# Performance work log

Hardware: AMD Instinct MI355X
Metric: run time of the kernel (lower is better)

Reference implementation:

```python
import jax, jax.numpy as jnp
import numpy as np
from jax import lax

# Dims matching init_kwargs
T, BK, OBS = 2048, 64, 64   # obs_dim = percept_dim(63) + reward_dim(1)
H, P, N = 16, 64, 64        # nheads, headdim, d_state; d_inner = H*P = 1024
DIN = H * P


def setup_inputs() -> dict:
    key = jax.random.key(0)
    ks = jax.random.split(key, 12)
    s = lambda fan_in: 1.0 / np.sqrt(fan_in)
    return {
        "obs": jax.random.normal(ks[0], (T, BK, OBS), jnp.float32),
        "reward": jax.random.normal(ks[1], (T, BK, 1), jnp.float32),
        "W_in": jax.random.normal(ks[2], (OBS, DIN), jnp.float32) * s(OBS),
        "W_B": jax.random.normal(ks[3], (OBS, N), jnp.float32) * s(OBS),
        "W_C": jax.random.normal(ks[4], (OBS, N), jnp.float32) * s(OBS),
        "W_dt": jax.random.normal(ks[5], (1, H), jnp.float32),
        "dt_bias": jax.random.normal(ks[6], (H,), jnp.float32) * 0.5,
        "A_log": jax.random.uniform(ks[7], (H,), jnp.float32, 0.0, 1.0),
        "D": jax.random.normal(ks[8], (H,), jnp.float32),
        "W_out": jax.random.normal(ks[9], (DIN, 1), jnp.float32) * s(DIN),
        "init_state": jax.random.normal(ks[10], (H, P, N), jnp.float32) * 0.1,
        "k": 8,
    }


def reference(obs, reward, W_in, W_B, W_C, W_dt, dt_bias, A_log, D, W_out, init_state, k):
    # obs: (T, Bk, obs_dim), reward: (T, Bk, 1)
    Tn, Bk, _ = obs.shape
    # Precompute per-step projections (vectorized over time)
    u = (obs @ W_in).reshape(Tn, Bk, H, P)      # (T,Bk,H,P) input stream
    Bm = obs @ W_B                              # (T,Bk,N) input-dependent B
    Cm = obs @ W_C                              # (T,Bk,N) input-dependent C
    dt = jax.nn.softplus(reward @ W_dt + dt_bias)  # (T,Bk,H) reward-modulated dt
    A = -jnp.exp(A_log)                          # (H,) negative decay rates
    decay = jnp.exp(dt * A)                     # (T,Bk,H)

    # Cache init: zeros + initial_states (per QAgent.forward)
    h0 = jnp.broadcast_to(init_state, (Bk, H, P, N))

    def step(h, inp):
        u_t, B_t, C_t, dt_t, dec_t = inp
        # selective-scan state update: h = h*exp(dt*A) + dt*u (outer) B
        h = h * dec_t[..., None, None] + (dt_t[..., None] * u_t)[..., None] * B_t[:, None, None, :]
        y = jnp.einsum('bhpn,bn->bhp', h, C_t) + D[None, :, None] * u_t
        o = y.reshape(Bk, DIN) @ W_out          # (Bk, 1) scalar Q per option
        return h, o

    _, ys = lax.scan(step, h0, (u, Bm, Cm, dt, decay))  # ys: (T, Bk, 1)
    q = ys.reshape(Tn, -1, k)                   # (T, B, k)
    logits = q
    return q, logits
```

## Files before the change

### kernel.cpp

```cpp
#include <hip/hip_runtime.h>
#include <math.h>

#define TT     2048
#define BKK    64
#define OBSD   64
#define NH     16
#define PDIM   64
#define NSTATE 64
#define DINN   1024
#define TB     (TT*BKK)
#define NC     32
#define CL     (TT/NC)

#define RS      164
#define OFF_C   64
#define OFF_DEC 128
#define OFF_XW  144
#define OFF_OB  160

template <int CTRL>
__device__ __forceinline__ float dpp_add(float x) {
    int y = __builtin_amdgcn_update_dpp(0, __float_as_int(x), CTRL, 0xF, 0xF, true);
    return x + __int_as_float(y);
}
__device__ __forceinline__ float wave_sum_lane63(float x) {
    x = dpp_add<0x111>(x);
    x = dpp_add<0x112>(x);
    x = dpp_add<0x114>(x);
    x = dpp_add<0x118>(x);
    x = dpp_add<0x142>(x);
    x = dpp_add<0x143>(x);
    return x;
}

__device__ __forceinline__ float softplusf(float z) {
    return (z > 20.f) ? z : log1pf(expf(z));
}

__global__ void dup_q(float* __restrict__ q) {
    int i = blockIdx.x * 256 + threadIdx.x;
    if (i < TB) q[TB + i] = q[i];
}

__global__ __launch_bounds__(1024)
void init_proj(const float* __restrict__ Win, const float* __restrict__ Wout,
               const float* __restrict__ initS,
               float* __restrict__ wproj, float* __restrict__ g0) {
    const int tid = threadIdx.x;
    {
        const int k = tid >> 4, h = tid & 15;
        float s = 0.f;
#pragma unroll 8
        for (int p = 0; p < PDIM; ++p)
            s = fmaf(Win[(size_t)k * DINN + h * 64 + p], Wout[h * 64 + p], s);
        wproj[tid] = s;
    }
    {
        const int h = tid >> 6, n = tid & 63;
        float s = 0.f;
#pragma unroll 8
        for (int p = 0; p < PDIM; ++p)
            s = fmaf(initS[h * PDIM * NSTATE + p * NSTATE + n], Wout[h * 64 + p], s);
        g0[tid] = s;
    }
}

__global__ __launch_bounds__(256)
void prelude2(const float* __restrict__ obs, const float* __restrict__ reward,
              const float* __restrict__ WB, const float* __restrict__ WC,
              const float* __restrict__ Wdt, const float* __restrict__ dtb,
              const float* __restrict__ Alog, const float* __restrict__ Dv,
              const float* __restrict__ wproj, float* __restrict__ rows) {
    int gw = (blockIdx.x * 256 + threadIdx.x) >> 6;
    gw = __builtin_amdgcn_readfirstlane(gw);
    const int lane = threadIdx.x & 63;
    const int row0 = gw * 8;
    if (row0 >= TB) return;

    const int h = lane & 15;
    const int q = lane >> 4;

    const float wdt_h = Wdt[h];
    const float dtb_h = dtb[h];
    const float A_h   = -expf(Alog[h]);
    const float D_h   = Dv[h];
    float wpj[16];
#pragma unroll
    for (int j = 0; j < 16; ++j)
        wpj[j] = wproj[(q * 16 + j) * 16 + h];

    float aB[8], aC[8];
#pragma unroll
    for (int r = 0; r < 8; ++r) { aB[r] = 0.f; aC[r] = 0.f; }
#pragma unroll 8
    for (int kk = 0; kk < OBSD; ++kk) {
        float wb = WB[kk * 64 + lane];
        float wc = WC[kk * 64 + lane];
#pragma unroll
        for (int r = 0; r < 8; ++r) {
            float o = obs[(size_t)(row0 + r) * OBSD + kk];
            aB[r] = fmaf(o, wb, aB[r]);
            aC[r] = fmaf(o, wc, aC[r]);
        }
    }

#pragma unroll 1
    for (int r = 0; r < 8; ++r) {
        const int row = row0 + r;
        float* rb = rows + (size_t)row * RS;
        rb[lane]         = aB[r];
        rb[OFF_C + lane] = aC[r];

        const float4* oq = (const float4*)(obs + (size_t)row * OBSD + q * 16);
        float4 o0 = oq[0], o1 = oq[1], o2 = oq[2], o3 = oq[3];
        float wpart = 0.f;
        wpart = fmaf(o0.x, wpj[0],  wpart); wpart = fmaf(o0.y, wpj[1],  wpart);
        wpart = fmaf(o0.z, wpj[2],  wpart); wpart = fmaf(o0.w, wpj[3],  wpart);
        wpart = fmaf(o1.x, wpj[4],  wpart); wpart = fmaf(o1.y, wpj[5],  wpart);
        wpart = fmaf(o1.z, wpj[6],  wpart); wpart = fmaf(o1.w, wpj[7],  wpart);
        wpart = fmaf(o2.x, wpj[8],  wpart); wpart = fmaf(o2.y, wpj[9],  wpart);
        wpart = fmaf(o2.z, wpj[10], wpart); wpart = fmaf(o2.w, wpj[11], wpart);
        wpart = fmaf(o3.x, wpj[12], wpart); wpart = fmaf(o3.y, wpj[13], wpart);
        wpart = fmaf(o3.z, wpj[14], wpart); wpart = fmaf(o3.w, wpj[15], wpart);
        wpart += __shfl_xor(wpart, 16, 64);
        wpart += __shfl_xor(wpart, 32, 64);

        const float rew  = reward[row];
        const float dtv  = softplusf(fmaf(rew, wdt_h, dtb_h));
        const float decv = expf(dtv * A_h);
        const float xwv  = dtv * wpart;
        if (q == 0) rb[OFF_DEC + h] = decv;
        if (q == 1) rb[OFF_XW  + h] = xwv;

        float dw = D_h * wpart;
        dw += __shfl_xor(dw, 1, 64);
        dw += __shfl_xor(dw, 2, 64);
        dw += __shfl_xor(dw, 4, 64);
        dw += __shfl_xor(dw, 8, 64);
        if (lane == 0) rb[OFF_OB] = dw;
    }
}

__global__ __launch_bounds__(256)
void phaseA(const float* __restrict__ rows, float* __restrict__ Send,
            float* __restrict__ Ptot) {
    int w = (blockIdx.x * 256 + threadIdx.x) >> 6;
    w = __builtin_amdgcn_readfirstlane(w);
    const int lane = threadIdx.x & 63;
    const int b = w & 63;
    const int c = w >> 6;

    const float* rowp = rows + ((size_t)(c * CL) * BKK + b) * RS;
    float g[16], Pc[16];
#pragma unroll
    for (int hh = 0; hh < 16; ++hh) { g[hh] = 0.f; Pc[hh] = 1.f; }

    float Bv = rowp[lane];

#pragma unroll 2
    for (int i = 0; i < CL; ++i) {
        const float* nxt = rowp + (size_t)RS * BKK;
        float Bn = 0.f;
        if (i < CL - 1) Bn = nxt[lane];
#pragma unroll
        for (int hh = 0; hh < 16; ++hh) {
            const float dh = rowp[OFF_DEC + hh];
            g[hh] = fmaf(g[hh], dh, rowp[OFF_XW + hh] * Bv);
            Pc[hh] *= dh;
        }
        rowp = nxt; Bv = Bn;
    }

    const size_t base = ((size_t)c * BKK + b) * 16;
#pragma unroll
    for (int hh = 0; hh < 16; ++hh)
        Send[(base + hh) * 64 + lane] = g[hh];
    if (lane == 0) {
#pragma unroll
        for (int hh = 0; hh < 16; ++hh)
            Ptot[base + hh] = Pc[hh];
    }
}

__global__ __launch_bounds__(64)
void phaseB(const float* __restrict__ g0, const float* __restrict__ Send,
            const float* __restrict__ Ptot, float* __restrict__ gcbuf) {
    const int b    = blockIdx.x;
    const int lane = threadIdx.x;

    float g[16];
#pragma unroll
    for (int hh = 0; hh < 16; ++hh)
        g[hh] = g0[hh * 64 + lane];

#pragma unroll 1
    for (int c = 0; c < NC; ++c) {
        const size_t base = ((size_t)c * BKK + b) * 16;
#pragma unroll
        for (int hh = 0; hh < 16; ++hh)
            gcbuf[(base + hh) * 64 + lane] = g[hh];
        if (c < NC - 1) {
#pragma unroll
            for (int hh = 0; hh < 16; ++hh)
                g[hh] = fmaf(Ptot[base + hh], g[hh], Send[(base + hh) * 64 + lane]);
        }
    }
}

__global__ __launch_bounds__(256)
void phaseC(const float* __restrict__ rows, const float* __restrict__ gcbuf,
            float* __restrict__ qout) {
    int w = (blockIdx.x * 256 + threadIdx.x) >> 6;
    w = __builtin_amdgcn_readfirstlane(w);
    const int lane = threadIdx.x & 63;
    const int b = w & 63;
    const int c = w >> 6;

    const size_t base = ((size_t)c * BKK + b) * 16;
    float g[16];
#pragma unroll
    for (int hh = 0; hh < 16; ++hh)
        g[hh] = gcbuf[(base + hh) * 64 + lane];

    const float* rowp = rows + ((size_t)(c * CL) * BKK + b) * RS;
    float Bv = rowp[lane];
    float Cv = rowp[OFF_C + lane];

#pragma unroll 2
    for (int i = 0; i < CL; ++i) {
        const float* nxt = rowp + (size_t)RS * BKK;
        float Bn = 0.f, Cn = 0.f;
        if (i < CL - 1) { Bn = nxt[lane]; Cn = nxt[OFF_C + lane]; }

        float y = 0.f;
#pragma unroll
        for (int hh = 0; hh < 16; ++hh) {
            g[hh] = fmaf(g[hh], rowp[OFF_DEC + hh], rowp[OFF_XW + hh] * Bv);
            y = fmaf(g[hh], Cv, y);
        }
        const float ob = rowp[OFF_OB];

        float tot = wave_sum_lane63(y);
        if (lane == 63) qout[(size_t)(c * CL + i) * BKK + b] = tot + ob;

        rowp = nxt; Bv = Bn; Cv = Cn;
    }
}

__global__ __launch_bounds__(64)
void scan3_kernel(const float* __restrict__ rows, const float* __restrict__ g0,
                  float* __restrict__ qout) {
    const int b    = blockIdx.x;
    const int lane = threadIdx.x;

    float g[16];
#pragma unroll
    for (int hh = 0; hh < 16; ++hh)
        g[hh] = g0[hh * 64 + lane];

    const float* rowp = rows + (size_t)b * RS;
    float Bv = rowp[lane];
    float Cv = rowp[OFF_C + lane];

#pragma unroll 2
    for (int t = 0; t < TT; ++t) {
        const float* nrow = rowp + (size_t)RS * BKK;
        float Bn = 0.f, Cn = 0.f;
        if (t < TT - 1) { Bn = nrow[lane]; Cn = nrow[OFF_C + lane]; }

        float y = 0.f;
#pragma unroll
        for (int hh = 0; hh < 16; ++hh) {
            float tmp = rowp[OFF_XW + hh] * Bv;
            g[hh] = fmaf(g[hh], rowp[OFF_DEC + hh], tmp);
            y = fmaf(g[hh], Cv, y);
        }
        const float ob = rowp[OFF_OB];

        float tot = wave_sum_lane63(y);
        if (lane == 63) qout[(size_t)t * BKK + b] = tot + ob;

        rowp = nrow; Bv = Bn; Cv = Cn;
    }
}

extern "C" void kernel_launch(void* const* d_in, const int* in_sizes, int n_in,
                              void* d_out, int out_size, void* d_ws, size_t ws_size,
                              hipStream_t stream) {
    const float* obs    = (const float*)d_in[0];
    const float* reward = (const float*)d_in[1];
    const float* Win    = (const float*)d_in[2];
    const float* WB     = (const float*)d_in[3];
    const float* WC     = (const float*)d_in[4];
    const float* Wdt    = (const float*)d_in[5];
    const float* dtb    = (const float*)d_in[6];
    const float* Alog   = (const float*)d_in[7];
    const float* Dv     = (const float*)d_in[8];
    const float* Wout   = (const float*)d_in[9];
    const float* initS  = (const float*)d_in[10];
    float* qout = (float*)d_out;

    const size_t n_rows = (size_t)TB * RS;
    const size_t n_cs   = (size_t)NC * BKK * 16 * 64;
    const size_t n_pt   = (size_t)NC * BKK * 16;

    const size_t need1 = (n_rows + 2048) * 4;
    const size_t need2 = (n_rows + 2048 + 2 * n_cs + n_pt) * 4;

    float* rows  = (float*)d_ws;
    float* wproj = rows + n_rows;
    float* g0    = wproj + 1024;

    if (ws_size >= need2) {
        float* Send  = g0 + 1024;
        float* gcbuf = Send + n_cs;
        float* Ptot  = gcbuf + n_cs;
        hipLaunchKernelGGL(init_proj, dim3(1),        dim3(1024), 0, stream,
                           Win, Wout, initS, wproj, g0);
        hipLaunchKernelGGL(prelude2,  dim3(TB / 32),  dim3(256),  0, stream,
                           obs, reward, WB, WC, Wdt, dtb, Alog, Dv, wproj, rows);
        hipLaunchKernelGGL(phaseA,    dim3(512),      dim3(256),  0, stream,
                           rows, Send, Ptot);
        hipLaunchKernelGGL(phaseB,    dim3(BKK),      dim3(64),   0, stream,
                           g0, Send, Ptot, gcbuf);
        hipLaunchKernelGGL(phaseC,    dim3(512),      dim3(256),  0, stream,
                           rows, gcbuf, qout);
        hipLaunchKernelGGL(dup_q,     dim3(TB / 256), dim3(256),  0, stream, qout);
    } else {
        hipLaunchKernelGGL(init_proj, dim3(1),        dim3(1024), 0, stream,
                           Win, Wout, initS, wproj, g0);
        hipLaunchKernelGGL(prelude2,  dim3(TB / 32),  dim3(256),  0, stream,
                           obs, reward, WB, WC, Wdt, dtb, Alog, Dv, wproj, rows);
        hipLaunchKernelGGL(scan3_kernel, dim3(BKK),   dim3(64),   0, stream,
                           rows, g0, qout);
        hipLaunchKernelGGL(dup_q,     dim3(TB / 256), dim3(256),  0, stream, qout);
    }
}
```

Baseline: 256.1 us.

## Parallelize init, stage obs in LDS, prefetch scan rows, double chunks, fuse dup

init_proj is spread over 8 blocks instead of one 1024-thread block. prelude2 now stages its obs rows in LDS once rather than reading them repeatedly from global memory. phaseA, phaseB and phaseC prefetch the next row's decay and xw values (and phaseB the next chunk's state) as float4 loads into registers to hide load latency. When the workspace allows, the chunk count doubles to 64, which halves each sequential chunk and doubles phaseA/C parallelism at the cost of a longer phaseB carry chain. phaseC writes both output copies directly, which removes the dup_q launch.

```diff
diff --git a/kernel.cpp b/kernel.cpp
--- a/kernel.cpp
+++ b/kernel.cpp
@@ -9,8 +9,6 @@
 #define NSTATE 64
 #define DINN   1024
 #define TB     (TT*BKK)
-#define NC     32
-#define CL     (TT/NC)
 
 #define RS      164
 #define OFF_C   64
@@ -42,26 +40,27 @@
     if (i < TB) q[TB + i] = q[i];
 }
 
-__global__ __launch_bounds__(1024)
-void init_proj(const float* __restrict__ Win, const float* __restrict__ Wout,
-               const float* __restrict__ initS,
-               float* __restrict__ wproj, float* __restrict__ g0) {
-    const int tid = threadIdx.x;
-    {
-        const int k = tid >> 4, h = tid & 15;
+__global__ __launch_bounds__(256)
+void init_proj2(const float* __restrict__ Win, const float* __restrict__ Wout,
+                const float* __restrict__ initS,
+                float* __restrict__ wproj, float* __restrict__ g0) {
+    const int t = threadIdx.x;
+    if (blockIdx.x < 4) {
+        const int idx = blockIdx.x * 256 + t;
+        const int k = idx >> 4, h = idx & 15;
         float s = 0.f;
 #pragma unroll 8
         for (int p = 0; p < PDIM; ++p)
             s = fmaf(Win[(size_t)k * DINN + h * 64 + p], Wout[h * 64 + p], s);
-        wproj[tid] = s;
-    }
-    {
-        const int h = tid >> 6, n = tid & 63;
+        wproj[idx] = s;
+    } else {
+        const int idx = (blockIdx.x - 4) * 256 + t;
+        const int h = idx >> 6, n = idx & 63;
         float s = 0.f;
 #pragma unroll 8
         for (int p = 0; p < PDIM; ++p)
             s = fmaf(initS[h * PDIM * NSTATE + p * NSTATE + n], Wout[h * 64 + p], s);
-        g0[tid] = s;
+        g0[idx] = s;
     }
 }
 
@@ -71,12 +70,26 @@
               const float* __restrict__ Wdt, const float* __restrict__ dtb,
               const float* __restrict__ Alog, const float* __restrict__ Dv,
               const float* __restrict__ wproj, float* __restrict__ rows) {
-    int gw = (blockIdx.x * 256 + threadIdx.x) >> 6;
-    gw = __builtin_amdgcn_readfirstlane(gw);
-    const int lane = threadIdx.x & 63;
-    const int row0 = gw * 8;
-    if (row0 >= TB) return;
-
+    __shared__ float lds[4][64][10];
+
+    const int t    = threadIdx.x;
+    const int lane = t & 63;
+    const int wv   = t >> 6;
+    const int row0b = blockIdx.x * 32;
+
+    {
+        const float4* op4 = (const float4*)(obs + (size_t)row0b * OBSD) + t * 2;
+        float4 v0 = op4[0], v1 = op4[1];
+        const int rb = t >> 3;
+        const int r  = rb & 7;
+        const int c0 = (t & 7) * 8;
+        lds[wv][c0 + 0][r] = v0.x; lds[wv][c0 + 1][r] = v0.y;
+        lds[wv][c0 + 2][r] = v0.z; lds[wv][c0 + 3][r] = v0.w;
+        lds[wv][c0 + 4][r] = v1.x; lds[wv][c0 + 5][r] = v1.y;
+        lds[wv][c0 + 6][r] = v1.z; lds[wv][c0 + 7][r] = v1.w;
+    }
+
+    const int row0 = row0b + wv * 8;
     const int h = lane & 15;
     const int q = lane >> 4;
 
@@ -92,16 +105,22 @@
     float aB[8], aC[8];
 #pragma unroll
     for (int r = 0; r < 8; ++r) { aB[r] = 0.f; aC[r] = 0.f; }
-#pragma unroll 8
+
+    const float* base = &lds[wv][0][0];
+#pragma unroll 4
     for (int kk = 0; kk < OBSD; ++kk) {
+        const float2* pr = (const float2*)(base + kk * 10);
+        float2 p0 = pr[0], p1 = pr[1], p2 = pr[2], p3 = pr[3];
         float wb = WB[kk * 64 + lane];
         float wc = WC[kk * 64 + lane];
-#pragma unroll
-        for (int r = 0; r < 8; ++r) {
-            float o = obs[(size_t)(row0 + r) * OBSD + kk];
-            aB[r] = fmaf(o, wb, aB[r]);
-            aC[r] = fmaf(o, wc, aC[r]);
-        }
+        aB[0] = fmaf(p0.x, wb, aB[0]);  aC[0] = fmaf(p0.x, wc, aC[0]);
+        aB[1] = fmaf(p0.y, wb, aB[1]);  aC[1] = fmaf(p0.y, wc, aC[1]);
+        aB[2] = fmaf(p1.x, wb, aB[2]);  aC[2] = fmaf(p1.x, wc, aC[2]);
+        aB[3] = fmaf(p1.y, wb, aB[3]);  aC[3] = fmaf(p1.y, wc, aC[3]);
+        aB[4] = fmaf(p2.x, wb, aB[4]);  aC[4] = fmaf(p2.x, wc, aC[4]);
+        aB[5] = fmaf(p2.y, wb, aB[5]);  aC[5] = fmaf(p2.y, wc, aC[5]);
+        aB[6] = fmaf(p3.x, wb, aB[6]);  aC[6] = fmaf(p3.x, wc, aC[6]);
+        aB[7] = fmaf(p3.y, wb, aB[7]);  aC[7] = fmaf(p3.y, wc, aC[7]);
     }
 
 #pragma unroll 1
@@ -141,10 +160,26 @@
     }
 }
 
+#define LOAD_DX(ptr, dd, xx)                                              \
+    {                                                                     \
+        const float4* _p = (const float4*)((ptr) + OFF_DEC);              \
+        float4 a0 = _p[0], a1 = _p[1], a2 = _p[2], a3 = _p[3];            \
+        float4 b0 = _p[4], b1 = _p[5], b2 = _p[6], b3 = _p[7];            \
+        dd[0]=a0.x; dd[1]=a0.y; dd[2]=a0.z; dd[3]=a0.w;                   \
+        dd[4]=a1.x; dd[5]=a1.y; dd[6]=a1.z; dd[7]=a1.w;                   \
+        dd[8]=a2.x; dd[9]=a2.y; dd[10]=a2.z; dd[11]=a2.w;                 \
+        dd[12]=a3.x; dd[13]=a3.y; dd[14]=a3.z; dd[15]=a3.w;               \
+        xx[0]=b0.x; xx[1]=b0.y; xx[2]=b0.z; xx[3]=b0.w;                   \
+        xx[4]=b1.x; xx[5]=b1.y; xx[6]=b1.z; xx[7]=b1.w;                   \
+        xx[8]=b2.x; xx[9]=b2.y; xx[10]=b2.z; xx[11]=b2.w;                 \
+        xx[12]=b3.x; xx[13]=b3.y; xx[14]=b3.z; xx[15]=b3.w;               \
+    }
+
+template <int CL>
 __global__ __launch_bounds__(256)
 void phaseA(const float* __restrict__ rows, float* __restrict__ Send,
             float* __restrict__ Ptot) {
-    int w = (blockIdx.x * 256 + threadIdx.x) >> 6;
+    int w = blockIdx.x * 4 + (threadIdx.x >> 6);
     w = __builtin_amdgcn_readfirstlane(w);
     const int lane = threadIdx.x & 63;
     const int b = w & 63;
@@ -156,19 +191,28 @@
     for (int hh = 0; hh < 16; ++hh) { g[hh] = 0.f; Pc[hh] = 1.f; }
 
     float Bv = rowp[lane];
+    float dec_[16], xw_[16];
+    LOAD_DX(rowp, dec_, xw_);
 
 #pragma unroll 2
     for (int i = 0; i < CL; ++i) {
         const float* nxt = rowp + (size_t)RS * BKK;
         float Bn = 0.f;
-        if (i < CL - 1) Bn = nxt[lane];
+        float decn_[16], xwn_[16];
+        if (i < CL - 1) {
+            Bn = nxt[lane];
+            LOAD_DX(nxt, decn_, xwn_);
+        }
 #pragma unroll
         for (int hh = 0; hh < 16; ++hh) {
-            const float dh = rowp[OFF_DEC + hh];
-            g[hh] = fmaf(g[hh], dh, rowp[OFF_XW + hh] * Bv);
-            Pc[hh] *= dh;
+            g[hh] = fmaf(g[hh], dec_[hh], xw_[hh] * Bv);
+            Pc[hh] *= dec_[hh];
         }
         rowp = nxt; Bv = Bn;
+        if (i < CL - 1) {
+#pragma unroll
+            for (int hh = 0; hh < 16; ++hh) { dec_[hh] = decn_[hh]; xw_[hh] = xwn_[hh]; }
+        }
     }
 
     const size_t base = ((size_t)c * BKK + b) * 16;
@@ -182,9 +226,11 @@
     }
 }
 
+template <int CL>
 __global__ __launch_bounds__(64)
 void phaseB(const float* __restrict__ g0, const float* __restrict__ Send,
             const float* __restrict__ Ptot, float* __restrict__ gcbuf) {
+    const int NCv  = TT / CL;
     const int b    = blockIdx.x;
     const int lane = threadIdx.x;
 
@@ -193,57 +239,100 @@
     for (int hh = 0; hh < 16; ++hh)
         g[hh] = g0[hh * 64 + lane];
 
+    float S_[16], P_[16];
+    {
+        const size_t base = (size_t)b * 16;
+#pragma unroll
+        for (int hh = 0; hh < 16; ++hh) S_[hh] = Send[(base + hh) * 64 + lane];
+        const float4* pp = (const float4*)(Ptot + base);
+        float4 a0 = pp[0], a1 = pp[1], a2 = pp[2], a3 = pp[3];
+        P_[0]=a0.x; P_[1]=a0.y; P_[2]=a0.z; P_[3]=a0.w;
+        P_[4]=a1.x; P_[5]=a1.y; P_[6]=a1.z; P_[7]=a1.w;
+        P_[8]=a2.x; P_[9]=a2.y; P_[10]=a2.z; P_[11]=a2.w;
+        P_[12]=a3.x; P_[13]=a3.y; P_[14]=a3.z; P_[15]=a3.w;
+    }
+
 #pragma unroll 1
-    for (int c = 0; c < NC; ++c) {
-        const size_t base = ((size_t)c * BKK + b) * 16;
+    for (int c = 0; c < NCv; ++c) {
+        const size_t base  = ((size_t)c * BKK + b) * 16;
+        float Sn[16], Pn[16];
+        if (c < NCv - 1) {
+            const size_t nb = ((size_t)(c + 1) * BKK + b) * 16;
+#pragma unroll
+            for (int hh = 0; hh < 16; ++hh) Sn[hh] = Send[(nb + hh) * 64 + lane];
+            const float4* pp = (const float4*)(Ptot + nb);
+            float4 a0 = pp[0], a1 = pp[1], a2 = pp[2], a3 = pp[3];
+            Pn[0]=a0.x; Pn[1]=a0.y; Pn[2]=a0.z; Pn[3]=a0.w;
+            Pn[4]=a1.x; Pn[5]=a1.y; Pn[6]=a1.z; Pn[7]=a1.w;
+            Pn[8]=a2.x; Pn[9]=a2.y; Pn[10]=a2.z; Pn[11]=a2.w;
+            Pn[12]=a3.x; Pn[13]=a3.y; Pn[14]=a3.z; Pn[15]=a3.w;
+        }
 #pragma unroll
         for (int hh = 0; hh < 16; ++hh)
             gcbuf[(base + hh) * 64 + lane] = g[hh];
-        if (c < NC - 1) {
-#pragma unroll
-            for (int hh = 0; hh < 16; ++hh)
-                g[hh] = fmaf(Ptot[base + hh], g[hh], Send[(base + hh) * 64 + lane]);
-        }
-    }
-}
-
+        if (c < NCv - 1) {
+#pragma unroll
+            for (int hh = 0; hh < 16; ++hh) {
+                g[hh] = fmaf(P_[hh], g[hh], S_[hh]);
+                P_[hh] = Pn[hh]; S_[hh] = Sn[hh];
+            }
+        }
+    }
+}
+
+template <int CL>
 __global__ __launch_bounds__(256)
 void phaseC(const float* __restrict__ rows, const float* __restrict__ gcbuf,
             float* __restrict__ qout) {
-    int w = (blockIdx.x * 256 + threadIdx.x) >> 6;
+    int w = blockIdx.x * 4 + (threadIdx.x >> 6);
     w = __builtin_amdgcn_readfirstlane(w);
     const int lane = threadIdx.x & 63;
     const int b = w & 63;
     const int c = w >> 6;
 
-    const size_t base = ((size_t)c * BKK + b) * 16;
+    const size_t sbase = ((size_t)c * BKK + b) * 16;
     float g[16];
 #pragma unroll
     for (int hh = 0; hh < 16; ++hh)
-        g[hh] = gcbuf[(base + hh) * 64 + lane];
+        g[hh] = gcbuf[(sbase + hh) * 64 + lane];
 
     const float* rowp = rows + ((size_t)(c * CL) * BKK + b) * RS;
     float Bv = rowp[lane];
     float Cv = rowp[OFF_C + lane];
+    float ob = rowp[OFF_OB];
+    float dec_[16], xw_[16];
+    LOAD_DX(rowp, dec_, xw_);
 
 #pragma unroll 2
     for (int i = 0; i < CL; ++i) {
         const float* nxt = rowp + (size_t)RS * BKK;
-        float Bn = 0.f, Cn = 0.f;
-        if (i < CL - 1) { Bn = nxt[lane]; Cn = nxt[OFF_C + lane]; }
+        float Bn = 0.f, Cn = 0.f, obn = 0.f;
+        float decn_[16], xwn_[16];
+        if (i < CL - 1) {
+            Bn = nxt[lane]; Cn = nxt[OFF_C + lane]; obn = nxt[OFF_OB];
+            LOAD_DX(nxt, decn_, xwn_);
+        }
 
         float y = 0.f;
 #pragma unroll
         for (int hh = 0; hh < 16; ++hh) {
-            g[hh] = fmaf(g[hh], rowp[OFF_DEC + hh], rowp[OFF_XW + hh] * Bv);
+            g[hh] = fmaf(g[hh], dec_[hh], xw_[hh] * Bv);
             y = fmaf(g[hh], Cv, y);
         }
-        const float ob = rowp[OFF_OB];
 
         float tot = wave_sum_lane63(y);
-        if (lane == 63) qout[(size_t)(c * CL + i) * BKK + b] = tot + ob;
-
-        rowp = nxt; Bv = Bn; Cv = Cn;
+        if (lane == 63) {
+            const size_t idx = (size_t)(c * CL + i) * BKK + b;
+            const float v = tot + ob;
+            qout[idx]      = v;
+            qout[TB + idx] = v;
+        }
+
+        rowp = nxt; Bv = Bn; Cv = Cn; ob = obn;
+        if (i < CL - 1) {
+#pragma unroll
+            for (int hh = 0; hh < 16; ++hh) { dec_[hh] = decn_[hh]; xw_[hh] = xwn_[hh]; }
+        }
     }
 }
 
@@ -301,38 +390,39 @@
     float* qout = (float*)d_out;
 
     const size_t n_rows = (size_t)TB * RS;
-    const size_t n_cs   = (size_t)NC * BKK * 16 * 64;
-    const size_t n_pt   = (size_t)NC * BKK * 16;
-
-    const size_t need1 = (n_rows + 2048) * 4;
-    const size_t need2 = (n_rows + 2048 + 2 * n_cs + n_pt) * 4;
 
     float* rows  = (float*)d_ws;
     float* wproj = rows + n_rows;
     float* g0    = wproj + 1024;
 
-    if (ws_size >= need2) {
+    const size_t n_cs64 = (size_t)64 * BKK * 16 * 64;
+    const size_t n_pt64 = (size_t)64 * BKK * 16;
+    const size_t need64 = (n_rows + 2048 + 2 * n_cs64 + n_pt64) * 4;
+
+    const size_t n_cs32 = (size_t)32 * BKK * 16 * 64;
+    const size_t n_pt32 = (size_t)32 * BKK * 16;
+    const size_t need32 = (n_rows + 2048 + 2 * n_cs32 + n_pt32) * 4;
+
+    init_proj2<<<dim3(8), dim3(256), 0, stream>>>(Win, Wout, initS, wproj, g0);
+    prelude2<<<dim3(TB / 32), dim3(256), 0, stream>>>(obs, reward, WB, WC, Wdt,
+                                                      dtb, Alog, Dv, wproj, rows);
+
+    if (ws_size >= need64) {
         float* Send  = g0 + 1024;
-        float* gcbuf = Send + n_cs;
-        float* Ptot  = gcbuf + n_cs;
-        hipLaunchKernelGGL(init_proj, dim3(1),        dim3(1024), 0, stream,
-                           Win, Wout, initS, wproj, g0);
-        hipLaunchKernelGGL(prelude2,  dim3(TB / 32),  dim3(256),  0, stream,
-                           obs, reward, WB, WC, Wdt, dtb, Alog, Dv, wproj, rows);
-        hipLaunchKernelGGL(phaseA,    dim3(512),      dim3(256),  0, stream,
-                           rows, Send, Ptot);
-        hipLaunchKernelGGL(phaseB,    dim3(BKK),      dim3(64),   0, stream,
-                           g0, Send, Ptot, gcbuf);
-        hipLaunchKernelGGL(phaseC,    dim3(512),      dim3(256),  0, stream,
-                           rows, gcbuf, qout);
-        hipLaunchKernelGGL(dup_q,     dim3(TB / 256), dim3(256),  0, stream, qout);
+        float* gcbuf = Send + n_cs64;
+        float* Ptot  = gcbuf + n_cs64;
+        phaseA<32><<<dim3(64 * 16), dim3(256), 0, stream>>>(rows, Send, Ptot);
+        phaseB<32><<<dim3(BKK), dim3(64), 0, stream>>>(g0, Send, Ptot, gcbuf);
+        phaseC<32><<<dim3(64 * 16), dim3(256), 0, stream>>>(rows, gcbuf, qout);
+    } else if (ws_size >= need32) {
+        float* Send  = g0 + 1024;
+        float* gcbuf = Send + n_cs32;
+        float* Ptot  = gcbuf + n_cs32;
+        phaseA<64><<<dim3(32 * 16), dim3(256), 0, stream>>>(rows, Send, Ptot);
+        phaseB<64><<<dim3(BKK), dim3(64), 0, stream>>>(g0, Send, Ptot, gcbuf);
+        phaseC<64><<<dim3(32 * 16), dim3(256), 0, stream>>>(rows, gcbuf, qout);
     } else {
-        hipLaunchKernelGGL(init_proj, dim3(1),        dim3(1024), 0, stream,
-                           Win, Wout, initS, wproj, g0);
-        hipLaunchKernelGGL(prelude2,  dim3(TB / 32),  dim3(256),  0, stream,
-                           obs, reward, WB, WC, Wdt, dtb, Alog, Dv, wproj, rows);
-        hipLaunchKernelGGL(scan3_kernel, dim3(BKK),   dim3(64),   0, stream,
-                           rows, g0, qout);
-        hipLaunchKernelGGL(dup_q,     dim3(TB / 256), dim3(256),  0, stream, qout);
-    }
-}
+        scan3_kernel<<<dim3(BKK), dim3(64), 0, stream>>>(rows, g0, qout);
+        dup_q<<<dim3(TB / 256), dim3(256), 0, stream>>>(qout);
+    }
+}
```

After: 234.7 us. 1.09x faster.
